# Kernel tuning notes

Measured on AMD Instinct MI355X. Metric: run time of the kernel, lower is better.

## Reference

```python
import jax, jax.numpy as jnp
import numpy as np

HEADS = 4
DIM_HEAD = 32


def setup_inputs() -> dict:
    key = jax.random.key(0)
    k1, k2, k3, k4 = jax.random.split(key, 4)
    dim = 256
    hidden = HEADS * DIM_HEAD  # 128
    B, N = 16, 8192
    x = jax.random.normal(k1, (B, dim, N), dtype=jnp.float32)
    # 1x1 conv weights squeezed to 2D matrices
    w_qkv = jax.random.normal(k2, (3 * hidden, dim), dtype=jnp.float32) * (dim ** -0.5)
    w_out = jax.random.normal(k3, (dim, hidden), dtype=jnp.float32) * (hidden ** -0.5)
    b_out = jax.random.normal(k4, (dim,), dtype=jnp.float32) * 0.01
    return {"x": x, "w_qkv": w_qkv, "w_out": w_out, "b_out": b_out}


def reference(x, w_qkv, w_out, b_out):
    # x: (B, C, N)
    B, C, N = x.shape
    hidden = HEADS * DIM_HEAD
    # 1x1 conv == channel GEMM: (B, 3*hidden, N)
    qkv = jnp.einsum('oc,bcn->bon', w_qkv, x)
    # split qkv and heads: (3, B, heads, dim_head, N)
    qkv = qkv.reshape(B, 3, HEADS, DIM_HEAD, N)
    q = qkv[:, 0]
    k = qkv[:, 1]
    v = qkv[:, 2]
    k = jax.nn.softmax(k, axis=-1)  # softmax over the N points
    # context: (B, heads, d, e) — tiny 32x32 per head
    context = jnp.einsum('bhdn,bhen->bhde', k, v)
    out = jnp.einsum('bhde,bhdn->bhen', context, q)  # (B, heads, d, N)
    out = out.reshape(B, hidden, N)
    out = jnp.einsum('oc,bcn->bon', w_out, out) + b_out[None, :, None]
    return out
```

## Files before the change

kernel.cpp:

```cpp
#include <hip/hip_runtime.h>
#include <hip/hip_bf16.h>
#include <math.h>

#define BB    16
#define CDIM  256
#define NN    8192
#define HEADS 4
#define DHEAD 32
#define HID   128
#define LDA   72

typedef __bf16 bf16x8 __attribute__((ext_vector_type(8)));
typedef float  f32x4  __attribute__((ext_vector_type(4)));

__device__ __forceinline__ unsigned short f2bf(float f) {
    union { float f; unsigned u; } v; v.f = f;
    unsigned u = v.u;
    return (unsigned short)((u + 0x7fffu + ((u >> 16) & 1u)) >> 16);
}

__global__ __launch_bounds__(256) void k_transpose(const float* __restrict__ x,
                                                   unsigned short* __restrict__ xt) {
    __shared__ __align__(16) unsigned short tile[64][68];
    int n0 = blockIdx.x * 64;
    int c0 = blockIdx.y * 64;
    int b  = blockIdx.z;
    const float* xb = x + (size_t)b * CDIM * NN;
    int t = threadIdx.x;
#pragma unroll
    for (int i = 0; i < 4; i++) {
        int idx  = t + 256 * i;
        int row  = idx >> 4;
        int col4 = (idx & 15) << 2;
        const float4 v = *(const float4*)(xb + (size_t)(c0 + row) * NN + n0 + col4);
        ushort4 o;
        o.x = f2bf(v.x); o.y = f2bf(v.y); o.z = f2bf(v.z); o.w = f2bf(v.w);
        *(ushort4*)&tile[row][col4] = o;
    }
    __syncthreads();
    unsigned short* xtb = xt + (size_t)b * NN * CDIM;
#pragma unroll
    for (int i = 0; i < 4; i++) {
        int idx  = t + 256 * i;
        int nrow = idx >> 4;
        int cg   = (idx & 15) << 2;
        ushort4 o;
        o.x = tile[cg + 0][nrow]; o.y = tile[cg + 1][nrow];
        o.z = tile[cg + 2][nrow]; o.w = tile[cg + 3][nrow];
        *(ushort4*)(xtb + (size_t)(n0 + nrow) * CDIM + c0 + cg) = o;
    }
}

__global__ __launch_bounds__(256) void k_convert_w(const float* __restrict__ w_qkv,
                                                   unsigned short* __restrict__ wkv) {
    int g = blockIdx.x * 256 + threadIdx.x;
    const float4 v = *(const float4*)(w_qkv + (size_t)HID * CDIM + (size_t)g * 4);
    ushort4 o;
    o.x = f2bf(v.x); o.y = f2bf(v.y); o.z = f2bf(v.z); o.w = f2bf(v.w);
    *(ushort4*)(wkv + (size_t)g * 4) = o;
}

__global__ __launch_bounds__(256) void k_qkv_ctx(const unsigned short* __restrict__ wkv,
                                                 const unsigned short* __restrict__ xt,
                                                 float* __restrict__ Cg,
                                                 float* __restrict__ Sg) {
    __shared__ __align__(16) unsigned short As[256 * LDA];
    __shared__ __align__(16) unsigned short Bs[64 * LDA];
    int n0 = blockIdx.x * 64;
    int b  = blockIdx.y;
    int t = threadIdx.x;
    int w = t >> 6, lane = t & 63, quad = lane >> 4, l16 = lane & 15;

    f32x4 acc[4][4];
#pragma unroll
    for (int i = 0; i < 4; i++)
#pragma unroll
        for (int j = 0; j < 4; j++) acc[i][j] = (f32x4){0.f, 0.f, 0.f, 0.f};

    const unsigned short* xb = xt + (size_t)b * NN * CDIM;

    for (int kt = 0; kt < 4; kt++) {
        int k0 = kt * 64;
#pragma unroll
        for (int i = 0; i < 8; i++) {
            int vid = t + 256 * i;
            int o   = vid >> 3;
            int kk  = (vid & 7) << 3;
            uint4 v = *(const uint4*)(wkv + (size_t)o * 256 + k0 + kk);
            *(uint4*)&As[o * LDA + kk] = v;
        }
#pragma unroll
        for (int i = 0; i < 2; i++) {
            int vid = t + 256 * i;
            int nl  = vid >> 3;
            int kk  = (vid & 7) << 3;
            uint4 v = *(const uint4*)(xb + (size_t)(n0 + nl) * CDIM + k0 + kk);
            *(uint4*)&Bs[nl * LDA + kk] = v;
        }
        __syncthreads();
#pragma unroll
        for (int kk = 0; kk < 64; kk += 32) {
            bf16x8 af[4], bfr[4];
#pragma unroll
            for (int mt = 0; mt < 4; mt++)
                af[mt] = *(const bf16x8*)&As[(w * 64 + mt * 16 + l16) * LDA + kk + quad * 8];
#pragma unroll
            for (int nt = 0; nt < 4; nt++)
                bfr[nt] = *(const bf16x8*)&Bs[(nt * 16 + l16) * LDA + kk + quad * 8];
#pragma unroll
            for (int mt = 0; mt < 4; mt++)
#pragma unroll
                for (int nt = 0; nt < 4; nt++)
                    acc[mt][nt] = __builtin_amdgcn_mfma_f32_16x16x32_bf16(af[mt], bfr[nt], acc[mt][nt], 0, 0, 0);
        }
        __syncthreads();
    }

    unsigned short* kvs = As;
    float sexp[4][4];
    bool isK = (w < 2);
#pragma unroll
    for (int mt = 0; mt < 4; mt++) {
#pragma unroll
        for (int reg = 0; reg < 4; reg++) {
            int o = w * 64 + mt * 16 + quad * 4 + reg;
            float s = 0.f;
#pragma unroll
            for (int nt = 0; nt < 4; nt++) {
                float v = acc[mt][nt][reg];
                if (isK) { v = __expf(v); s += v; }
                kvs[o * LDA + nt * 16 + l16] = f2bf(v);
            }
            sexp[mt][reg] = s;
        }
    }
    if (isK) {
#pragma unroll
        for (int mt = 0; mt < 4; mt++)
#pragma unroll
            for (int reg = 0; reg < 4; reg++) {
                float s = sexp[mt][reg];
                s += __shfl_xor(s, 1, 64);
                s += __shfl_xor(s, 2, 64);
                s += __shfl_xor(s, 4, 64);
                s += __shfl_xor(s, 8, 64);
                if (l16 == 0) {
                    int o = w * 64 + mt * 16 + quad * 4 + reg;
                    atomicAdd(&Sg[(b * HEADS + (o >> 5)) * DHEAD + (o & 31)], s);
                }
            }
    }
    __syncthreads();

    {
        int h = w;
        f32x4 cacc[2][2];
#pragma unroll
        for (int i = 0; i < 2; i++)
#pragma unroll
            for (int j = 0; j < 2; j++) cacc[i][j] = (f32x4){0.f, 0.f, 0.f, 0.f};
#pragma unroll
        for (int nk = 0; nk < 64; nk += 32) {
            bf16x8 pa[2], vb[2];
#pragma unroll
            for (int dt = 0; dt < 2; dt++)
                pa[dt] = *(const bf16x8*)&kvs[(h * 32 + dt * 16 + l16) * LDA + nk + quad * 8];
#pragma unroll
            for (int et = 0; et < 2; et++)
                vb[et] = *(const bf16x8*)&kvs[(128 + h * 32 + et * 16 + l16) * LDA + nk + quad * 8];
#pragma unroll
            for (int dt = 0; dt < 2; dt++)
#pragma unroll
                for (int et = 0; et < 2; et++)
                    cacc[dt][et] = __builtin_amdgcn_mfma_f32_16x16x32_bf16(pa[dt], vb[et], cacc[dt][et], 0, 0, 0);
        }
        float* Cb = Cg + (size_t)(b * HEADS + h) * 32 * 32;
#pragma unroll
        for (int dt = 0; dt < 2; dt++)
#pragma unroll
            for (int et = 0; et < 2; et++)
#pragma unroll
                for (int reg = 0; reg < 4; reg++) {
                    int d = dt * 16 + quad * 4 + reg;
                    int e = et * 16 + l16;
                    atomicAdd(&Cb[d * 32 + e], cacc[dt][et][reg]);
                }
    }
}

__global__ __launch_bounds__(256) void k_build_m(const float* __restrict__ w_out,
                                                 const float* __restrict__ w_qkv,
                                                 const float* __restrict__ Cg,
                                                 const float* __restrict__ Sg,
                                                 unsigned short* __restrict__ Mb) {
    __shared__ float Arow[16][128];
    int ot = blockIdx.x;
    int b  = blockIdx.y;
    int t  = threadIdx.x;
    const float* Cb = Cg + (size_t)b * HEADS * 32 * 32;
    const float* Sb = Sg + (size_t)b * HEADS * 32;
#pragma unroll
    for (int i = 0; i < 8; i++) {
        int ent = t + 256 * i;
        int ol  = ent >> 7;
        int hd  = ent & 127;
        int h = hd >> 5, d = hd & 31;
        const float* wo = w_out + (size_t)(ot * 16 + ol) * HID + h * 32;
        const float* cc = Cb + (h * 32 + d) * 32;
        float s = 0.f;
#pragma unroll
        for (int e = 0; e < 32; e++) s += wo[e] * cc[e];
        Arow[ol][hd] = s / Sb[h * 32 + d];
    }
    __syncthreads();
    unsigned short* Mo = Mb + (size_t)b * CDIM * CDIM;
#pragma unroll
    for (int i = 0; i < 16; i++) {
        int ol = i;
        int c  = t;
        float s = 0.f;
#pragma unroll 8
        for (int hd = 0; hd < 128; hd++) s += Arow[ol][hd] * w_qkv[(size_t)hd * CDIM + c];
        Mo[(size_t)(ot * 16 + ol) * CDIM + c] = f2bf(s);
    }
}

__global__ __launch_bounds__(256) void k_out_gemm(const unsigned short* __restrict__ Mb,
                                                  const unsigned short* __restrict__ xt,
                                                  const float* __restrict__ b_out,
                                                  float* __restrict__ out) {
    __shared__ __align__(16) unsigned short As[256 * LDA];
    __shared__ __align__(16) unsigned short Bs[64 * LDA];
    int n0 = blockIdx.x * 64;
    int b  = blockIdx.y;
    int t = threadIdx.x;
    int w = t >> 6, lane = t & 63, quad = lane >> 4, l16 = lane & 15;

    f32x4 acc[4][4];
#pragma unroll
    for (int i = 0; i < 4; i++)
#pragma unroll
        for (int j = 0; j < 4; j++) acc[i][j] = (f32x4){0.f, 0.f, 0.f, 0.f};

    const unsigned short* Ab = Mb + (size_t)b * CDIM * CDIM;
    const unsigned short* xb = xt + (size_t)b * NN * CDIM;

    for (int kt = 0; kt < 4; kt++) {
        int k0 = kt * 64;
#pragma unroll
        for (int i = 0; i < 8; i++) {
            int vid = t + 256 * i;
            int o   = vid >> 3;
            int kk  = (vid & 7) << 3;
            uint4 v = *(const uint4*)(Ab + (size_t)o * 256 + k0 + kk);
            *(uint4*)&As[o * LDA + kk] = v;
        }
#pragma unroll
        for (int i = 0; i < 2; i++) {
            int vid = t + 256 * i;
            int nl  = vid >> 3;
            int kk  = (vid & 7) << 3;
            uint4 v = *(const uint4*)(xb + (size_t)(n0 + nl) * CDIM + k0 + kk);
            *(uint4*)&Bs[nl * LDA + kk] = v;
        }
        __syncthreads();
#pragma unroll
        for (int kk = 0; kk < 64; kk += 32) {
            bf16x8 af[4], bfr[4];
#pragma unroll
            for (int mt = 0; mt < 4; mt++)
                af[mt] = *(const bf16x8*)&As[(w * 64 + mt * 16 + l16) * LDA + kk + quad * 8];
#pragma unroll
            for (int nt = 0; nt < 4; nt++)
                bfr[nt] = *(const bf16x8*)&Bs[(nt * 16 + l16) * LDA + kk + quad * 8];
#pragma unroll
            for (int mt = 0; mt < 4; mt++)
#pragma unroll
                for (int nt = 0; nt < 4; nt++)
                    acc[mt][nt] = __builtin_amdgcn_mfma_f32_16x16x32_bf16(af[mt], bfr[nt], acc[mt][nt], 0, 0, 0);
        }
        __syncthreads();
    }

    float* ob = out + (size_t)b * CDIM * NN;
#pragma unroll
    for (int mt = 0; mt < 4; mt++)
#pragma unroll
        for (int reg = 0; reg < 4; reg++) {
            int o = w * 64 + mt * 16 + quad * 4 + reg;
            float bo = b_out[o];
#pragma unroll
            for (int nt = 0; nt < 4; nt++)
                ob[(size_t)o * NN + n0 + nt * 16 + l16] = acc[mt][nt][reg] + bo;
        }
}

extern "C" void kernel_launch(void* const* d_in, const int* in_sizes, int n_in,
                              void* d_out, int out_size, void* d_ws, size_t ws_size,
                              hipStream_t stream) {
    const float* x     = (const float*)d_in[0];
    const float* w_qkv = (const float*)d_in[1];
    const float* w_out = (const float*)d_in[2];
    const float* b_out = (const float*)d_in[3];
    float* out = (float*)d_out;

    char* ws = (char*)d_ws;
    const size_t off_xt  = 0;
    const size_t off_wkv = off_xt + 67108864;
    const size_t off_C   = off_wkv + 131072;
    const size_t off_S   = off_C + 262144;
    const size_t off_M   = off_S + 8192;

    unsigned short* xt  = (unsigned short*)(ws + off_xt);
    unsigned short* wkv = (unsigned short*)(ws + off_wkv);
    float*          Cg  = (float*)(ws + off_C);
    float*          Sg  = (float*)(ws + off_S);
    unsigned short* Mb  = (unsigned short*)(ws + off_M);

    hipMemsetAsync(Cg, 0, 262144 + 8192, stream);
    k_transpose<<<dim3(NN / 64, CDIM / 64, BB), 256, 0, stream>>>(x, xt);
    k_convert_w<<<dim3(64), 256, 0, stream>>>(w_qkv, wkv);
    k_qkv_ctx<<<dim3(NN / 64, BB), 256, 0, stream>>>(wkv, xt, Cg, Sg);
    k_build_m<<<dim3(16, BB), 256, 0, stream>>>(w_out, w_qkv, Cg, Sg, Mb);
    k_out_gemm<<<dim3(NN / 64, BB), 256, 0, stream>>>(Mb, xt, b_out, out);
}
```

Measured before the change: 454.5 us.

## Replace atomic context accumulation with per-slot partials and a reduction kernel

k_qkv_ctx now has each block process four 64-point chunks and accumulate the context and exp sums in registers. Each block writes its partial results to a per-slot buffer instead of issuing global atomicAdds. A new k_reduce kernel sums the 32 slots and stores reciprocal softmax denominators, which removes the memset and lets k_build_m multiply instead of divide. The grid shrinks from 2048 to 512 blocks, which lowers occupancy and parallelism on a large GPU, and it adds a kernel launch plus partial-buffer traffic.

```diff
diff --git a/kernel.cpp b/kernel.cpp
--- a/kernel.cpp
+++ b/kernel.cpp
@@ -2,13 +2,15 @@
 #include <hip/hip_bf16.h>
 #include <math.h>
 
-#define BB    16
-#define CDIM  256
-#define NN    8192
-#define HEADS 4
-#define DHEAD 32
-#define HID   128
-#define LDA   72
+#define BB     16
+#define CDIM   256
+#define NN     8192
+#define HEADS  4
+#define DHEAD  32
+#define HID    128
+#define LDA    72
+#define NCHUNK 256
+#define SLOTS  32
 
 typedef __bf16 bf16x8 __attribute__((ext_vector_type(8)));
 typedef float  f32x4  __attribute__((ext_vector_type(4)));
@@ -62,143 +64,173 @@
 
 __global__ __launch_bounds__(256) void k_qkv_ctx(const unsigned short* __restrict__ wkv,
                                                  const unsigned short* __restrict__ xt,
-                                                 float* __restrict__ Cg,
-                                                 float* __restrict__ Sg) {
+                                                 float* __restrict__ Cpart,
+                                                 float* __restrict__ Spart) {
     __shared__ __align__(16) unsigned short As[256 * LDA];
     __shared__ __align__(16) unsigned short Bs[64 * LDA];
-    int n0 = blockIdx.x * 64;
-    int b  = blockIdx.y;
+    int slot = blockIdx.x;
+    int b    = blockIdx.y;
     int t = threadIdx.x;
     int w = t >> 6, lane = t & 63, quad = lane >> 4, l16 = lane & 15;
-
-    f32x4 acc[4][4];
+    bool isK = (w < 2);
+
+    f32x4 cacc[2][2];
+#pragma unroll
+    for (int i = 0; i < 2; i++)
+#pragma unroll
+        for (int j = 0; j < 2; j++) cacc[i][j] = (f32x4){0.f, 0.f, 0.f, 0.f};
+    float sexpA[4][4];
 #pragma unroll
     for (int i = 0; i < 4; i++)
 #pragma unroll
-        for (int j = 0; j < 4; j++) acc[i][j] = (f32x4){0.f, 0.f, 0.f, 0.f};
+        for (int j = 0; j < 4; j++) sexpA[i][j] = 0.f;
 
     const unsigned short* xb = xt + (size_t)b * NN * CDIM;
-
-    for (int kt = 0; kt < 4; kt++) {
-        int k0 = kt * 64;
-#pragma unroll
-        for (int i = 0; i < 8; i++) {
-            int vid = t + 256 * i;
-            int o   = vid >> 3;
-            int kk  = (vid & 7) << 3;
-            uint4 v = *(const uint4*)(wkv + (size_t)o * 256 + k0 + kk);
-            *(uint4*)&As[o * LDA + kk] = v;
-        }
-#pragma unroll
-        for (int i = 0; i < 2; i++) {
-            int vid = t + 256 * i;
-            int nl  = vid >> 3;
-            int kk  = (vid & 7) << 3;
-            uint4 v = *(const uint4*)(xb + (size_t)(n0 + nl) * CDIM + k0 + kk);
-            *(uint4*)&Bs[nl * LDA + kk] = v;
+    unsigned short* kvs = As;
+
+    for (int s = 0; s < 4; s++) {
+        int n0 = slot * NCHUNK + s * 64;
+
+        f32x4 acc[4][4];
+#pragma unroll
+        for (int i = 0; i < 4; i++)
+#pragma unroll
+            for (int j = 0; j < 4; j++) acc[i][j] = (f32x4){0.f, 0.f, 0.f, 0.f};
+
+        for (int kt = 0; kt < 4; kt++) {
+            int k0 = kt * 64;
+#pragma unroll
+            for (int i = 0; i < 8; i++) {
+                int vid = t + 256 * i;
+                int o   = vid >> 3;
+                int kk  = (vid & 7) << 3;
+                uint4 v = *(const uint4*)(wkv + (size_t)o * 256 + k0 + kk);
+                *(uint4*)&As[o * LDA + kk] = v;
+            }
+#pragma unroll
+            for (int i = 0; i < 2; i++) {
+                int vid = t + 256 * i;
+                int nl  = vid >> 3;
+                int kk  = (vid & 7) << 3;
+                uint4 v = *(const uint4*)(xb + (size_t)(n0 + nl) * CDIM + k0 + kk);
+                *(uint4*)&Bs[nl * LDA + kk] = v;
+            }
+            __syncthreads();
+#pragma unroll
+            for (int kk = 0; kk < 64; kk += 32) {
+                bf16x8 af[4], bfr[4];
+#pragma unroll
+                for (int mt = 0; mt < 4; mt++)
+                    af[mt] = *(const bf16x8*)&As[(w * 64 + mt * 16 + l16) * LDA + kk + quad * 8];
+#pragma unroll
+                for (int nt = 0; nt < 4; nt++)
+                    bfr[nt] = *(const bf16x8*)&Bs[(nt * 16 + l16) * LDA + kk + quad * 8];
+#pragma unroll
+                for (int mt = 0; mt < 4; mt++)
+#pragma unroll
+                    for (int nt = 0; nt < 4; nt++)
+                        acc[mt][nt] = __builtin_amdgcn_mfma_f32_16x16x32_bf16(af[mt], bfr[nt], acc[mt][nt], 0, 0, 0);
+            }
+            __syncthreads();
+        }
+
+#pragma unroll
+        for (int mt = 0; mt < 4; mt++) {
+#pragma unroll
+            for (int reg = 0; reg < 4; reg++) {
+                int o = w * 64 + mt * 16 + quad * 4 + reg;
+#pragma unroll
+                for (int nt = 0; nt < 4; nt++) {
+                    float v = acc[mt][nt][reg];
+                    if (isK) { v = __expf(v); sexpA[mt][reg] += v; }
+                    kvs[o * LDA + nt * 16 + l16] = f2bf(v);
+                }
+            }
         }
         __syncthreads();
-#pragma unroll
-        for (int kk = 0; kk < 64; kk += 32) {
-            bf16x8 af[4], bfr[4];
-#pragma unroll
-            for (int mt = 0; mt < 4; mt++)
-                af[mt] = *(const bf16x8*)&As[(w * 64 + mt * 16 + l16) * LDA + kk + quad * 8];
-#pragma unroll
-            for (int nt = 0; nt < 4; nt++)
-                bfr[nt] = *(const bf16x8*)&Bs[(nt * 16 + l16) * LDA + kk + quad * 8];
-#pragma unroll
-            for (int mt = 0; mt < 4; mt++)
-#pragma unroll
-                for (int nt = 0; nt < 4; nt++)
-                    acc[mt][nt] = __builtin_amdgcn_mfma_f32_16x16x32_bf16(af[mt], bfr[nt], acc[mt][nt], 0, 0, 0);
+
+        {
+            int h = w;
+#pragma unroll
+            for (int nk = 0; nk < 64; nk += 32) {
+                bf16x8 pa[2], vb[2];
+#pragma unroll
+                for (int dt = 0; dt < 2; dt++)
+                    pa[dt] = *(const bf16x8*)&kvs[(h * 32 + dt * 16 + l16) * LDA + nk + quad * 8];
+#pragma unroll
+                for (int et = 0; et < 2; et++)
+                    vb[et] = *(const bf16x8*)&kvs[(128 + h * 32 + et * 16 + l16) * LDA + nk + quad * 8];
+#pragma unroll
+                for (int dt = 0; dt < 2; dt++)
+#pragma unroll
+                    for (int et = 0; et < 2; et++)
+                        cacc[dt][et] = __builtin_amdgcn_mfma_f32_16x16x32_bf16(pa[dt], vb[et], cacc[dt][et], 0, 0, 0);
+            }
         }
         __syncthreads();
     }
 
-    unsigned short* kvs = As;
-    float sexp[4][4];
-    bool isK = (w < 2);
-#pragma unroll
-    for (int mt = 0; mt < 4; mt++) {
-#pragma unroll
-        for (int reg = 0; reg < 4; reg++) {
-            int o = w * 64 + mt * 16 + quad * 4 + reg;
-            float s = 0.f;
-#pragma unroll
-            for (int nt = 0; nt < 4; nt++) {
-                float v = acc[mt][nt][reg];
-                if (isK) { v = __expf(v); s += v; }
-                kvs[o * LDA + nt * 16 + l16] = f2bf(v);
-            }
-            sexp[mt][reg] = s;
-        }
-    }
+    float* Cb = Cpart + ((size_t)(b * SLOTS + slot) * HEADS + w) * 1024;
+#pragma unroll
+    for (int dt = 0; dt < 2; dt++)
+#pragma unroll
+        for (int et = 0; et < 2; et++)
+#pragma unroll
+            for (int reg = 0; reg < 4; reg++) {
+                int d = dt * 16 + quad * 4 + reg;
+                int e = et * 16 + l16;
+                Cb[d * 32 + e] = cacc[dt][et][reg];
+            }
     if (isK) {
 #pragma unroll
         for (int mt = 0; mt < 4; mt++)
 #pragma unroll
             for (int reg = 0; reg < 4; reg++) {
-                float s = sexp[mt][reg];
+                float s = sexpA[mt][reg];
                 s += __shfl_xor(s, 1, 64);
                 s += __shfl_xor(s, 2, 64);
                 s += __shfl_xor(s, 4, 64);
                 s += __shfl_xor(s, 8, 64);
                 if (l16 == 0) {
                     int o = w * 64 + mt * 16 + quad * 4 + reg;
-                    atomicAdd(&Sg[(b * HEADS + (o >> 5)) * DHEAD + (o & 31)], s);
+                    Spart[((size_t)b * SLOTS + slot) * 128 + o] = s;
                 }
             }
     }
-    __syncthreads();
-
-    {
-        int h = w;
-        f32x4 cacc[2][2];
-#pragma unroll
-        for (int i = 0; i < 2; i++)
-#pragma unroll
-            for (int j = 0; j < 2; j++) cacc[i][j] = (f32x4){0.f, 0.f, 0.f, 0.f};
-#pragma unroll
-        for (int nk = 0; nk < 64; nk += 32) {
-            bf16x8 pa[2], vb[2];
-#pragma unroll
-            for (int dt = 0; dt < 2; dt++)
-                pa[dt] = *(const bf16x8*)&kvs[(h * 32 + dt * 16 + l16) * LDA + nk + quad * 8];
-#pragma unroll
-            for (int et = 0; et < 2; et++)
-                vb[et] = *(const bf16x8*)&kvs[(128 + h * 32 + et * 16 + l16) * LDA + nk + quad * 8];
-#pragma unroll
-            for (int dt = 0; dt < 2; dt++)
-#pragma unroll
-                for (int et = 0; et < 2; et++)
-                    cacc[dt][et] = __builtin_amdgcn_mfma_f32_16x16x32_bf16(pa[dt], vb[et], cacc[dt][et], 0, 0, 0);
-        }
-        float* Cb = Cg + (size_t)(b * HEADS + h) * 32 * 32;
-#pragma unroll
-        for (int dt = 0; dt < 2; dt++)
-#pragma unroll
-            for (int et = 0; et < 2; et++)
-#pragma unroll
-                for (int reg = 0; reg < 4; reg++) {
-                    int d = dt * 16 + quad * 4 + reg;
-                    int e = et * 16 + l16;
-                    atomicAdd(&Cb[d * 32 + e], cacc[dt][et][reg]);
-                }
+}
+
+__global__ __launch_bounds__(256) void k_reduce(const float* __restrict__ Cpart,
+                                                const float* __restrict__ Spart,
+                                                float* __restrict__ Cg,
+                                                float* __restrict__ Sinv) {
+    int q = blockIdx.x, h = blockIdx.y, b = blockIdx.z;
+    int t = threadIdx.x;
+    int e = q * 256 + t;
+    float acc = 0.f;
+#pragma unroll 4
+    for (int sl = 0; sl < SLOTS; sl++)
+        acc += Cpart[((size_t)(b * SLOTS + sl) * HEADS + h) * 1024 + e];
+    Cg[((size_t)b * HEADS + h) * 1024 + e] = acc;
+    if (q == 0 && t < 32) {
+        float s = 0.f;
+#pragma unroll 4
+        for (int sl = 0; sl < SLOTS; sl++)
+            s += Spart[((size_t)b * SLOTS + sl) * 128 + h * 32 + t];
+        Sinv[((size_t)b * HEADS + h) * 32 + t] = 1.0f / s;
     }
 }
 
 __global__ __launch_bounds__(256) void k_build_m(const float* __restrict__ w_out,
                                                  const float* __restrict__ w_qkv,
                                                  const float* __restrict__ Cg,
-                                                 const float* __restrict__ Sg,
+                                                 const float* __restrict__ Sinv,
                                                  unsigned short* __restrict__ Mb) {
     __shared__ float Arow[16][128];
     int ot = blockIdx.x;
     int b  = blockIdx.y;
     int t  = threadIdx.x;
     const float* Cb = Cg + (size_t)b * HEADS * 32 * 32;
-    const float* Sb = Sg + (size_t)b * HEADS * 32;
+    const float* Sb = Sinv + (size_t)b * HEADS * 32;
 #pragma unroll
     for (int i = 0; i < 8; i++) {
         int ent = t + 256 * i;
@@ -210,7 +242,7 @@
         float s = 0.f;
 #pragma unroll
         for (int e = 0; e < 32; e++) s += wo[e] * cc[e];
-        Arow[ol][hd] = s / Sb[h * 32 + d];
+        Arow[ol][hd] = s * Sb[h * 32 + d];
     }
     __syncthreads();
     unsigned short* Mo = Mb + (size_t)b * CDIM * CDIM;
@@ -305,22 +337,26 @@
     float* out = (float*)d_out;
 
     char* ws = (char*)d_ws;
-    const size_t off_xt  = 0;
-    const size_t off_wkv = off_xt + 67108864;
-    const size_t off_C   = off_wkv + 131072;
-    const size_t off_S   = off_C + 262144;
-    const size_t off_M   = off_S + 8192;
-
-    unsigned short* xt  = (unsigned short*)(ws + off_xt);
-    unsigned short* wkv = (unsigned short*)(ws + off_wkv);
-    float*          Cg  = (float*)(ws + off_C);
-    float*          Sg  = (float*)(ws + off_S);
-    unsigned short* Mb  = (unsigned short*)(ws + off_M);
-
-    hipMemsetAsync(Cg, 0, 262144 + 8192, stream);
+    const size_t off_xt    = 0;
+    const size_t off_wkv   = off_xt + 67108864;
+    const size_t off_Cpart = off_wkv + 131072;
+    const size_t off_Spart = off_Cpart + 8388608;
+    const size_t off_Cg    = off_Spart + 262144;
+    const size_t off_Sinv  = off_Cg + 262144;
+    const size_t off_M     = off_Sinv + 8192;
+
+    unsigned short* xt    = (unsigned short*)(ws + off_xt);
+    unsigned short* wkv   = (unsigned short*)(ws + off_wkv);
+    float*          Cpart = (float*)(ws + off_Cpart);
+    float*          Spart = (float*)(ws + off_Spart);
+    float*          Cg    = (float*)(ws + off_Cg);
+    float*          Sinv  = (float*)(ws + off_Sinv);
+    unsigned short* Mb    = (unsigned short*)(ws + off_M);
+
     k_transpose<<<dim3(NN / 64, CDIM / 64, BB), 256, 0, stream>>>(x, xt);
     k_convert_w<<<dim3(64), 256, 0, stream>>>(w_qkv, wkv);
-    k_qkv_ctx<<<dim3(NN / 64, BB), 256, 0, stream>>>(wkv, xt, Cg, Sg);
-    k_build_m<<<dim3(16, BB), 256, 0, stream>>>(w_out, w_qkv, Cg, Sg, Mb);
+    k_qkv_ctx<<<dim3(SLOTS, BB), 256, 0, stream>>>(wkv, xt, Cpart, Spart);
+    k_reduce<<<dim3(4, HEADS, BB), 256, 0, stream>>>(Cpart, Spart, Cg, Sinv);
+    k_build_m<<<dim3(16, BB), 256, 0, stream>>>(w_out, w_qkv, Cg, Sinv, Mb);
     k_out_gemm<<<dim3(NN / 64, BB), 256, 0, stream>>>(Mb, xt, b_out, out);
 }
```

Measured after the change: 389.7 us. 1.17x faster.
